# Kernel optimization log

Measured on AMD Instinct MI355X. Metric: run time of the kernel, lower is better.

Reference implementation:

```python
import jax, jax.numpy as jnp
import numpy as np

N_NODES = 100000


def _gcn_conv(x, W, b, src, dst, deg_inv_sqrt, n):
    # PyG GCNConv: h = x @ W; out[i] = sum_{(j->i)} norm_ji * h[j] + b
    h = x @ W                                   # [N, out_dim]
    norm = deg_inv_sqrt[src] * deg_inv_sqrt[dst]  # [E_total]
    msg = h[src] * norm[:, None]                # gather + scale
    out = jax.ops.segment_sum(msg, dst, num_segments=n)  # scatter-add
    return out + b


def setup_inputs() -> dict:
    key = jax.random.key(0)
    k1, k2, k3, k4, k5, k6 = jax.random.split(key, 6)
    num_features, hidden, embedding_size = 128, 32, 64
    n_edges = 3200000
    x = jax.random.normal(k1, (N_NODES, num_features), dtype=jnp.float32)
    edge_index = jax.random.randint(k2, (2, n_edges), 0, N_NODES, dtype=jnp.int64)
    # Glorot init like PyG GCNConv
    W1 = jax.random.normal(k3, (num_features, hidden), dtype=jnp.float32) * (1.0 / np.sqrt(num_features))
    b1 = jnp.zeros((hidden,), dtype=jnp.float32)
    W2 = jax.random.normal(k4, (hidden, embedding_size), dtype=jnp.float32) * (1.0 / np.sqrt(hidden))
    b2 = jnp.zeros((embedding_size,), dtype=jnp.float32)
    return {"x": x, "edge_index": edge_index, "W1": W1, "b1": b1, "W2": W2, "b2": b2}


def reference(x, edge_index, W1, b1, W2, b2):
    n = x.shape[0]
    # add self-loops (GCNConv default add_self_loops=True)
    loop = jnp.arange(n, dtype=edge_index.dtype)
    src = jnp.concatenate([edge_index[0], loop])
    dst = jnp.concatenate([edge_index[1], loop])
    # symmetric normalization: deg includes self-loops, edge_weight = 1
    deg = jax.ops.segment_sum(jnp.ones_like(dst, dtype=x.dtype), dst, num_segments=n)
    deg_inv_sqrt = jnp.where(deg > 0, jax.lax.rsqrt(deg), 0.0)

    h = _gcn_conv(x, W1, b1, src, dst, deg_inv_sqrt, n)
    h = jax.nn.relu(h)
    # F.dropout(p=0.2, training=False) -> identity in eval mode
    out = _gcn_conv(h, W2, b2, src, dst, deg_inv_sqrt, n)
    return out
```

## Files before the change

kernel.cpp:

```cpp
#include <hip/hip_runtime.h>
#include <hip/hip_bf16.h>


#define NF 128
#define HID 32
#define EMB 64

#define BSHIFT 10
#define BNODES 1024
#define CAPS 4608
#define CAP (8 * CAPS)
#define NBUKMAX 128
#define TILE 4096
#define EPT 16
#define CHUNKS 8

typedef float vf4 __attribute__((ext_vector_type(4)));
typedef unsigned vu4 __attribute__((ext_vector_type(4)));

static __device__ __forceinline__ unsigned bf16rne(float f) {
    unsigned u = __float_as_uint(f);
    return (u + 0x7fffu + ((u >> 16) & 1u)) >> 16;
}

static __device__ __host__ __forceinline__ int hslot(int b, int c) {
    return ((b >> 3) << 6) | (c << 3) | (b & 7);
}

#define ACC8(v) \
    a0 += __uint_as_float((v).x << 16); a1 += __uint_as_float((v).x & 0xffff0000u); \
    a2 += __uint_as_float((v).y << 16); a3 += __uint_as_float((v).y & 0xffff0000u); \
    a4 += __uint_as_float((v).z << 16); a5 += __uint_as_float((v).z & 0xffff0000u); \
    a6 += __uint_as_float((v).w << 16); a7 += __uint_as_float((v).w & 0xffff0000u);

__global__ __launch_bounds__(256) void k_part(const void* __restrict__ ei,
                                              unsigned* __restrict__ pairs,
                                              int* __restrict__ bcur8,
                                              int* __restrict__ cnt_ovf,
                                              unsigned long long* __restrict__ ovf,
                                              int* __restrict__ ovfcnt,
                                              int E, int nbuk) {
    __shared__ unsigned sEnt[TILE];
    __shared__ unsigned char sB[TILE];
    __shared__ int hcntw[4][NBUKMAX];
    __shared__ int lcurw[4][NBUKMAX];
    __shared__ int lstart[NBUKMAX], gbase[NBUKMAX];
    __shared__ int sNZ;
    const int tid = threadIdx.x;
    const int w = tid >> 6;
    const int grp = blockIdx.x & 7;
    const int tile0 = blockIdx.x * TILE;
    if (tile0 >= E) return;
    const int tcnt = min(TILE, E - tile0);

    if (tid == 0) sNZ = 0;
    for (int b = tid; b < 4 * NBUKMAX; b += 256) {
        ((int*)hcntw)[b] = 0;
        ((int*)lcurw)[b] = 0;
    }
    __syncthreads();
    {
        int i = tile0 + tid;
        if (i < E) {
            unsigned hw = ((const unsigned*)ei)[2 * (size_t)i + 1];
            if (hw) sNZ = 1;
        }
    }
    __syncthreads();
    const bool is64 = (sNZ == 0);

    int ms[EPT], md[EPT];
#pragma unroll
    for (int k = 0; k < EPT; ++k) {
        int i = tile0 + k * 256 + tid;
        ms[k] = -1;
        if (i < tile0 + tcnt) {
            int s, d;
            if (is64) {
                const long long* p = (const long long*)ei;
                s = (int)__builtin_nontemporal_load(&p[i]);
                d = (int)__builtin_nontemporal_load(&p[(size_t)E + i]);
            } else {
                const int* p = (const int*)ei;
                s = __builtin_nontemporal_load(&p[i]);
                d = __builtin_nontemporal_load(&p[E + i]);
            }
            ms[k] = s; md[k] = d;
            atomicAdd(&hcntw[w][d >> BSHIFT], 1);
        }
    }
    __syncthreads();

    if (tid < 64) {
        int i0 = tid * 2, i1 = tid * 2 + 1;
        int c0 = 0, c1 = 0;
        if (i0 < nbuk) { c0 = hcntw[0][i0] + hcntw[1][i0] + hcntw[2][i0] + hcntw[3][i0]; }
        if (i1 < nbuk) { c1 = hcntw[0][i1] + hcntw[1][i1] + hcntw[2][i1] + hcntw[3][i1]; }
        int run = c0 + c1, inc = run;
#pragma unroll
        for (int off = 1; off < 64; off <<= 1) {
            int t2 = __shfl_up(inc, off);
            if (tid >= off) inc += t2;
        }
        int excl = inc - run;
        if (i0 < nbuk) {
            lstart[i0] = excl;
            gbase[i0] = c0 ? atomicAdd(&bcur8[i0 * 8 + grp], c0) : 0;
            int off2 = excl;
#pragma unroll
            for (int ww = 0; ww < 4; ++ww) { int t3 = hcntw[ww][i0]; hcntw[ww][i0] = off2; off2 += t3; }
        }
        if (i1 < nbuk) {
            lstart[i1] = excl + c0;
            gbase[i1] = c1 ? atomicAdd(&bcur8[i1 * 8 + grp], c1) : 0;
            int off2 = excl + c0;
#pragma unroll
            for (int ww = 0; ww < 4; ++ww) { int t3 = hcntw[ww][i1]; hcntw[ww][i1] = off2; off2 += t3; }
        }
    }
    __syncthreads();

#pragma unroll
    for (int k = 0; k < EPT; ++k) {
        if (ms[k] >= 0) {
            int b = md[k] >> BSHIFT;
            int slot = hcntw[w][b] + atomicAdd(&lcurw[w][b], 1);
            sEnt[slot] = ((unsigned)(md[k] & (BNODES - 1)) << 17) | (unsigned)ms[k];
            sB[slot] = (unsigned char)b;
        }
    }
    __syncthreads();

    for (int j = tid; j < tcnt; j += 256) {
        unsigned ent = sEnt[j];
        int b = sB[j];
        int g = gbase[b] + (j - lstart[b]);
        if (g < CAPS) {
            pairs[(size_t)b * CAP + grp * CAPS + g] = ent;
        } else {
            int d = (b << BSHIFT) | (int)(ent >> 17);
            int s = (int)(ent & 0x1FFFFu);
            int o = atomicAdd(ovfcnt, 1);
            ovf[o] = ((unsigned long long)(unsigned)d << 32) | (unsigned)s;
            atomicAdd(&cnt_ovf[d], 1);
        }
    }
}

__global__ void k_bscan(const int* __restrict__ bcur8, int* __restrict__ bbase,
                        int* __restrict__ roff, int nbuk, int E, int N) {
    __shared__ int sh[128];
    int t = threadIdx.x;
    int v = 0;
    if (t < nbuk) {
#pragma unroll
        for (int k = 0; k < 8; ++k) v += bcur8[t * 8 + k];
    }
    sh[t] = v;
    __syncthreads();
    for (int off = 1; off < 128; off <<= 1) {
        int add = (t >= off) ? sh[t - off] : 0;
        __syncthreads();
        sh[t] += add;
        __syncthreads();
    }
    if (t < nbuk) bbase[t] = sh[t] - v;
    if (t == 0) roff[N] = E;
}

__global__ __launch_bounds__(256) void k_hist(const unsigned* __restrict__ pairs,
                                              const int* __restrict__ bcur8,
                                              int* __restrict__ histc, int nbuk) {
    __shared__ int hist[BNODES];
    const int idx = blockIdx.x;
    const int c = (idx >> 3) & 7;
    const int b = (idx & 7) | ((idx >> 6) << 3);
    if (b >= nbuk) return;
    const int tid = threadIdx.x;
    const int nbc = min(bcur8[b * 8 + c], CAPS);
    const int i0 = c * CAPS, i1 = i0 + nbc;
    const unsigned* pp = pairs + (size_t)b * CAP;
    for (int i = tid; i < BNODES; i += 256) hist[i] = 0;
    __syncthreads();
    for (int i = i0 + tid; i < i1; i += 256)
        atomicAdd(&hist[__builtin_nontemporal_load(&pp[i]) >> 17], 1);
    __syncthreads();
    int* outp = histc + ((size_t)idx << 10);
    for (int i = tid; i < BNODES; i += 256) outp[i] = hist[i];
}

__global__ __launch_bounds__(256) void k_nscan(int* __restrict__ histc,
                                               const int* __restrict__ bbase,
                                               const int* __restrict__ cnt_ovf,
                                               int* __restrict__ roff,
                                               int* __restrict__ cursor,
                                               float* __restrict__ dis, int N) {
    __shared__ int part[256];
    const int b = blockIdx.x, tid = threadIdx.x;
    const int base = bbase[b];
    int h[4][CHUNKS], stg[4], tv[4];
    int run = 0;
    const int l0 = tid * 4;
#pragma unroll
    for (int k = 0; k < 4; ++k) {
        int l = l0 + k;
        int node = (b << BSHIFT) + l;
        int st = 0;
#pragma unroll
        for (int c = 0; c < CHUNKS; ++c) {
            h[k][c] = histc[((size_t)hslot(b, c) << 10) + l];
            st += h[k][c];
        }
        stg[k] = st;
        int ov = (node < N) ? cnt_ovf[node] : 0;
        tv[k] = st + ov;
        run += tv[k];
    }
    part[tid] = run;
    __syncthreads();
    for (int off = 1; off < 256; off <<= 1) {
        int add = (tid >= off) ? part[tid - off] : 0;
        __syncthreads();
        part[tid] += add;
        __syncthreads();
    }
    int excl = part[tid] - run;
#pragma unroll
    for (int k = 0; k < 4; ++k) {
        int l = l0 + k;
        int node = (b << BSHIFT) + l;
        if (node < N) {
            roff[node] = base + excl;
            cursor[node] = base + excl + stg[k];
            dis[node] = rsqrtf((float)(tv[k] + 1));
        }
        int cb = base + excl;
#pragma unroll
        for (int c = 0; c < CHUNKS; ++c) {
            int hh = h[k][c];
            histc[((size_t)hslot(b, c) << 10) + l] = cb;
            cb += hh;
        }
        excl += tv[k];
    }
}

__global__ __launch_bounds__(256) void k_scat2(const unsigned* __restrict__ pairs,
                                               const int* __restrict__ bcur8,
                                               const int* __restrict__ histc,
                                               int* __restrict__ csr,
                                               const unsigned long long* __restrict__ ovf,
                                               const int* __restrict__ ovfcnt,
                                               int* __restrict__ cursor, int nbuk) {
    __shared__ int cbase[BNODES];
    __shared__ int lc[BNODES];
    const int idx = blockIdx.x;
    const int c = (idx >> 3) & 7;
    const int b = (idx & 7) | ((idx >> 6) << 3);
    const int tid = threadIdx.x;
    if (b < nbuk) {
        const int nbc = min(bcur8[b * 8 + c], CAPS);
        const int i0 = c * CAPS, i1 = i0 + nbc;
        const unsigned* pp = pairs + (size_t)b * CAP;
        const int* hc = histc + ((size_t)idx << 10);
        for (int i = tid; i < BNODES; i += 256) { cbase[i] = hc[i]; lc[i] = 0; }
        __syncthreads();
        int i = i0 + tid;
        for (; i + 768 < i1; i += 1024) {
            unsigned e0 = pp[i], e1 = pp[i + 256], e2 = pp[i + 512], e3 = pp[i + 768];
            int l0 = e0 >> 17, l1 = e1 >> 17, l2 = e2 >> 17, l3 = e3 >> 17;
            int p0 = cbase[l0] + atomicAdd(&lc[l0], 1);
            int p1 = cbase[l1] + atomicAdd(&lc[l1], 1);
            int p2 = cbase[l2] + atomicAdd(&lc[l2], 1);
            int p3 = cbase[l3] + atomicAdd(&lc[l3], 1);
            csr[p0] = (int)(e0 & 0x1FFFFu);
            csr[p1] = (int)(e1 & 0x1FFFFu);
            csr[p2] = (int)(e2 & 0x1FFFFu);
            csr[p3] = (int)(e3 & 0x1FFFFu);
        }
        for (; i < i1; i += 256) {
            unsigned ent = pp[i];
            int l = ent >> 17;
            int pos = cbase[l] + atomicAdd(&lc[l], 1);
            csr[pos] = (int)(ent & 0x1FFFFu);
        }
    }
    int n = *ovfcnt;
    for (int i = idx * 256 + tid; i < n; i += gridDim.x * 256) {
        unsigned long long pr = ovf[i];
        int pos = atomicAdd(&cursor[(int)(unsigned)(pr >> 32)], 1);
        csr[pos] = (int)(unsigned)pr;
    }
}

__global__ __launch_bounds__(256) void k_gemm1(const float* __restrict__ x,
                                               const float* __restrict__ W,
                                               const float* __restrict__ dis,
                                               unsigned* __restrict__ h1b, int N) {
    __shared__ float sW[NF * HID];
    __shared__ float sx[32][132];
    const int t = threadIdx.x;
    for (int i = t; i < NF * HID; i += 256) sW[i] = W[i];
    const int row0 = blockIdx.x * 32;
    {
        const float4* xv = (const float4*)(x + (size_t)row0 * NF);
        for (int i = t; i < 32 * 32; i += 256) {
            int r = i >> 5, c = i & 31;
            float4 v = make_float4(0.f, 0.f, 0.f, 0.f);
            if (row0 + r < N) v = xv[(size_t)r * 32 + c];
            *(float4*)&sx[r][c * 4] = v;
        }
    }
    __syncthreads();
    const int col4 = (t & 7) * 4;
    const int row = t >> 3;
    float a0 = 0.f, a1 = 0.f, a2 = 0.f, a3 = 0.f;
#pragma unroll 8
    for (int k = 0; k < NF; ++k) {
        float xs = sx[row][k];
        float4 w = *(const float4*)&sW[k * HID + col4];
        a0 += xs * w.x; a1 += xs * w.y; a2 += xs * w.z; a3 += xs * w.w;
    }
    int r = row0 + row;
    if (r < N) {
        float d = dis[r];
        unsigned u0 = bf16rne(a0 * d) | (bf16rne(a1 * d) << 16);
        unsigned u1 = bf16rne(a2 * d) | (bf16rne(a3 * d) << 16);
        *(uint2*)&h1b[(size_t)r * 16 + (t & 7) * 2] = make_uint2(u0, u1);
    }
}

__global__ __launch_bounds__(256) void k_agg1(const uint4* __restrict__ h1b,
                                              const int* __restrict__ roff,
                                              const int* __restrict__ csr,
                                              const float* __restrict__ dis,
                                              const float* __restrict__ b1,
                                              uint4* __restrict__ t_out, int N) {
    int tt = blockIdx.x * 256 + threadIdx.x;
    int node = tt >> 2;
    if (node >= N) return;
    int j = tt & 3;
    uint4 u = h1b[(size_t)node * 4 + j];
    float a0, a1, a2, a3, a4, a5, a6, a7;
    a0 = __uint_as_float(u.x << 16); a1 = __uint_as_float(u.x & 0xffff0000u);
    a2 = __uint_as_float(u.y << 16); a3 = __uint_as_float(u.y & 0xffff0000u);
    a4 = __uint_as_float(u.z << 16); a5 = __uint_as_float(u.z & 0xffff0000u);
    a6 = __uint_as_float(u.w << 16); a7 = __uint_as_float(u.w & 0xffff0000u);
    int e0 = roff[node], e1 = roff[node + 1];
    int e = e0;
    for (; e + 8 <= e1; e += 8) {
        int s0 = __builtin_nontemporal_load(&csr[e + 0]);
        int s1 = __builtin_nontemporal_load(&csr[e + 1]);
        int s2 = __builtin_nontemporal_load(&csr[e + 2]);
        int s3 = __builtin_nontemporal_load(&csr[e + 3]);
        int s4 = __builtin_nontemporal_load(&csr[e + 4]);
        int s5 = __builtin_nontemporal_load(&csr[e + 5]);
        int s6 = __builtin_nontemporal_load(&csr[e + 6]);
        int s7 = __builtin_nontemporal_load(&csr[e + 7]);
        uint4 v0 = h1b[(size_t)s0 * 4 + j];
        uint4 v1 = h1b[(size_t)s1 * 4 + j];
        uint4 v2 = h1b[(size_t)s2 * 4 + j];
        uint4 v3 = h1b[(size_t)s3 * 4 + j];
        uint4 v4 = h1b[(size_t)s4 * 4 + j];
        uint4 v5 = h1b[(size_t)s5 * 4 + j];
        uint4 v6 = h1b[(size_t)s6 * 4 + j];
        uint4 v7 = h1b[(size_t)s7 * 4 + j];
        ACC8(v0) ACC8(v1) ACC8(v2) ACC8(v3) ACC8(v4) ACC8(v5) ACC8(v6) ACC8(v7)
    }
    for (; e + 4 <= e1; e += 4) {
        int s0 = __builtin_nontemporal_load(&csr[e + 0]);
        int s1 = __builtin_nontemporal_load(&csr[e + 1]);
        int s2 = __builtin_nontemporal_load(&csr[e + 2]);
        int s3 = __builtin_nontemporal_load(&csr[e + 3]);
        uint4 v0 = h1b[(size_t)s0 * 4 + j];
        uint4 v1 = h1b[(size_t)s1 * 4 + j];
        uint4 v2 = h1b[(size_t)s2 * 4 + j];
        uint4 v3 = h1b[(size_t)s3 * 4 + j];
        ACC8(v0) ACC8(v1) ACC8(v2) ACC8(v3)
    }
    for (; e < e1; ++e) {
        int s = __builtin_nontemporal_load(&csr[e]);
        uint4 v = h1b[(size_t)s * 4 + j];
        ACC8(v)
    }
    float d = dis[node];
    float4 bb0 = *(const float4*)&b1[j * 8];
    float4 bb1 = *(const float4*)&b1[j * 8 + 4];
    float r0 = fmaxf(a0 * d + bb0.x, 0.f) * d, r1 = fmaxf(a1 * d + bb0.y, 0.f) * d;
    float r2 = fmaxf(a2 * d + bb0.z, 0.f) * d, r3 = fmaxf(a3 * d + bb0.w, 0.f) * d;
    float r4 = fmaxf(a4 * d + bb1.x, 0.f) * d, r5 = fmaxf(a5 * d + bb1.y, 0.f) * d;
    float r6 = fmaxf(a6 * d + bb1.z, 0.f) * d, r7 = fmaxf(a7 * d + bb1.w, 0.f) * d;
    uint4 o;
    o.x = bf16rne(r0) | (bf16rne(r1) << 16);
    o.y = bf16rne(r2) | (bf16rne(r3) << 16);
    o.z = bf16rne(r4) | (bf16rne(r5) << 16);
    o.w = bf16rne(r6) | (bf16rne(r7) << 16);
    t_out[(size_t)node * 4 + j] = o;
}

__global__ __launch_bounds__(256) void k_agg2(const uint4* __restrict__ tb,
                                              const int* __restrict__ roff,
                                              const int* __restrict__ csr,
                                              const float* __restrict__ dis,
                                              float* __restrict__ s2, int N) {
    int tt = blockIdx.x * 256 + threadIdx.x;
    int node = tt >> 2;
    if (node >= N) return;
    int j = tt & 3;
    uint4 u = tb[(size_t)node * 4 + j];
    float a0, a1, a2, a3, a4, a5, a6, a7;
    a0 = __uint_as_float(u.x << 16); a1 = __uint_as_float(u.x & 0xffff0000u);
    a2 = __uint_as_float(u.y << 16); a3 = __uint_as_float(u.y & 0xffff0000u);
    a4 = __uint_as_float(u.z << 16); a5 = __uint_as_float(u.z & 0xffff0000u);
    a6 = __uint_as_float(u.w << 16); a7 = __uint_as_float(u.w & 0xffff0000u);
    int e0 = roff[node], e1 = roff[node + 1];
    int e = e0;
    for (; e + 8 <= e1; e += 8) {
        int s0 = __builtin_nontemporal_load(&csr[e + 0]);
        int s1 = __builtin_nontemporal_load(&csr[e + 1]);
        int s2i = __builtin_nontemporal_load(&csr[e + 2]);
        int s3 = __builtin_nontemporal_load(&csr[e + 3]);
        int s4 = __builtin_nontemporal_load(&csr[e + 4]);
        int s5 = __builtin_nontemporal_load(&csr[e + 5]);
        int s6 = __builtin_nontemporal_load(&csr[e + 6]);
        int s7 = __builtin_nontemporal_load(&csr[e + 7]);
        uint4 v0 = tb[(size_t)s0 * 4 + j];
        uint4 v1 = tb[(size_t)s1 * 4 + j];
        uint4 v2 = tb[(size_t)s2i * 4 + j];
        uint4 v3 = tb[(size_t)s3 * 4 + j];
        uint4 v4 = tb[(size_t)s4 * 4 + j];
        uint4 v5 = tb[(size_t)s5 * 4 + j];
        uint4 v6 = tb[(size_t)s6 * 4 + j];
        uint4 v7 = tb[(size_t)s7 * 4 + j];
        ACC8(v0) ACC8(v1) ACC8(v2) ACC8(v3) ACC8(v4) ACC8(v5) ACC8(v6) ACC8(v7)
    }
    for (; e + 4 <= e1; e += 4) {
        int s0 = __builtin_nontemporal_load(&csr[e + 0]);
        int s1 = __builtin_nontemporal_load(&csr[e + 1]);
        int s2i = __builtin_nontemporal_load(&csr[e + 2]);
        int s3 = __builtin_nontemporal_load(&csr[e + 3]);
        uint4 v0 = tb[(size_t)s0 * 4 + j];
        uint4 v1 = tb[(size_t)s1 * 4 + j];
        uint4 v2 = tb[(size_t)s2i * 4 + j];
        uint4 v3 = tb[(size_t)s3 * 4 + j];
        ACC8(v0) ACC8(v1) ACC8(v2) ACC8(v3)
    }
    for (; e < e1; ++e) {
        int s = __builtin_nontemporal_load(&csr[e]);
        uint4 v = tb[(size_t)s * 4 + j];
        ACC8(v)
    }
    float d = dis[node];
    vf4 o0, o1;
    o0.x = a0 * d; o0.y = a1 * d; o0.z = a2 * d; o0.w = a3 * d;
    o1.x = a4 * d; o1.y = a5 * d; o1.z = a6 * d; o1.w = a7 * d;
    vf4* op = (vf4*)&s2[(size_t)node * HID + j * 8];
    __builtin_nontemporal_store(o0, op);
    __builtin_nontemporal_store(o1, op + 1);
}

__global__ __launch_bounds__(256) void k_gemm2(const float* __restrict__ a,
                                               const float* __restrict__ W,
                                               const float* __restrict__ b2,
                                               float* __restrict__ out, int N) {
    __shared__ float sW[HID * EMB];
    __shared__ float sx[32][36];
    const int t = threadIdx.x;
    for (int i = t; i < HID * EMB; i += 256) sW[i] = W[i];
    const int row0 = blockIdx.x * 32;
    {
        const float4* av = (const float4*)(a + (size_t)row0 * HID);
        int r = t >> 3, c = t & 7;
        float4 v = make_float4(0.f, 0.f, 0.f, 0.f);
        if (row0 + r < N) v = av[(size_t)r * 8 + c];
        *(float4*)&sx[r][c * 4] = v;
    }
    __syncthreads();
    const int col4 = (t & 15) * 4;
    const int r0 = t >> 4;
    float a00 = 0.f, a01 = 0.f, a02 = 0.f, a03 = 0.f;
    float a10 = 0.f, a11 = 0.f, a12 = 0.f, a13 = 0.f;
#pragma unroll
    for (int k = 0; k < HID; ++k) {
        float4 w = *(const float4*)&sW[k * EMB + col4];
        float xa = sx[r0][k];
        float xb = sx[r0 + 16][k];
        a00 += xa * w.x; a01 += xa * w.y; a02 += xa * w.z; a03 += xa * w.w;
        a10 += xb * w.x; a11 += xb * w.y; a12 += xb * w.z; a13 += xb * w.w;
    }
    float4 bb = *(const float4*)&b2[col4];
    int ra = row0 + r0, rb = row0 + r0 + 16;
    if (ra < N) {
        vf4 o; o.x = a00 + bb.x; o.y = a01 + bb.y; o.z = a02 + bb.z; o.w = a03 + bb.w;
        __builtin_nontemporal_store(o, (vf4*)&out[(size_t)ra * EMB + col4]);
    }
    if (rb < N) {
        vf4 o; o.x = a10 + bb.x; o.y = a11 + bb.y; o.z = a12 + bb.z; o.w = a13 + bb.w;
        __builtin_nontemporal_store(o, (vf4*)&out[(size_t)rb * EMB + col4]);
    }
}

extern "C" void kernel_launch(void* const* d_in, const int* in_sizes, int n_in,
                              void* d_out, int out_size, void* d_ws, size_t ws_size,
                              hipStream_t stream) {
    const float* x  = (const float*)d_in[0];
    const void*  ei = d_in[1];
    const float* W1 = (const float*)d_in[2];
    const float* b1 = (const float*)d_in[3];
    const float* W2 = (const float*)d_in[4];
    const float* b2 = (const float*)d_in[5];
    float* out = (float*)d_out;

    const int N = in_sizes[0] / NF;
    const int E = in_sizes[1] / 2;
    const int nbuk = (N + BNODES - 1) >> BSHIFT;

    char* ws = (char*)d_ws;
    size_t off = 0;
    auto take = [&](size_t bytes) -> void* {
        void* p = ws + off;
        off += (bytes + 255) & ~(size_t)255;
        return p;
    };
    int* cnt_ovf = (int*)take((size_t)N * 4);
    int* bcur8   = (int*)take((size_t)NBUKMAX * 8 * 4);
    int* ovfcnt  = (int*)take(4);
    size_t zbytes = off;
    int*                bbase  = (int*)take((size_t)NBUKMAX * 4);
    int*                roff   = (int*)take((size_t)(N + 1) * 4);
    int*                cursor = (int*)take((size_t)N * 4);
    float*              dis    = (float*)take((size_t)N * 4);
    int*                histc  = (int*)take((size_t)NBUKMAX * CHUNKS * BNODES * 4);
    unsigned*           pairs  = (unsigned*)take((size_t)nbuk * CAP * 4);
    unsigned long long* ovf    = (unsigned long long*)take((size_t)E * 8);
    int*                csr    = (int*)take((size_t)E * 4);
    unsigned*           h1b    = (unsigned*)take((size_t)N * HID * 2);
    unsigned*           tb     = (unsigned*)take((size_t)N * HID * 2);
    float*              s2     = (float*)take((size_t)N * HID * 4);

    (void)hipMemsetAsync(cnt_ovf, 0, zbytes, stream);

    const int gridBC = ((nbuk + 7) / 8) * 64;
    const int gridAgg = (int)(((size_t)N * 4 + 255) / 256);

    k_part<<<(E + TILE - 1) / TILE, 256, 0, stream>>>(ei, pairs, bcur8, cnt_ovf,
                                                      ovf, ovfcnt, E, nbuk);
    k_bscan<<<1, 128, 0, stream>>>(bcur8, bbase, roff, nbuk, E, N);
    k_hist<<<gridBC, 256, 0, stream>>>(pairs, bcur8, histc, nbuk);
    k_nscan<<<nbuk, 256, 0, stream>>>(histc, bbase, cnt_ovf, roff, cursor, dis, N);
    k_scat2<<<gridBC, 256, 0, stream>>>(pairs, bcur8, histc, csr, ovf, ovfcnt,
                                        cursor, nbuk);

    k_gemm1<<<(N + 31) / 32, 256, 0, stream>>>(x, W1, dis, h1b, N);
    k_agg1<<<gridAgg, 256, 0, stream>>>((const uint4*)h1b, roff, csr, dis, b1,
                                        (uint4*)tb, N);
    k_agg2<<<gridAgg, 256, 0, stream>>>((const uint4*)tb, roff, csr, dis, s2, N);
    k_gemm2<<<(N + 31) / 32, 256, 0, stream>>>(s2, W2, b2, out, N);
}
```

Baseline: 231.6 us.

## Fuse second aggregation with output GEMM and simplify partition slot atomics

Merges the layer-2 aggregation kernel and the 32x64 output GEMM into one kernel. Aggregated rows are staged in shared memory and multiplied by W2 in the same block, which removes the s2 intermediate write and read and one launch. It also drops the separate lcurw counter array in the partition kernel by doing atomicAdd directly on the prefix-offset array. The fused kernel now loads W2 into shared memory in every aggregation block and adds a block barrier after the irregular gather loop.

```diff
diff --git a/kernel.cpp b/kernel.cpp
--- a/kernel.cpp
+++ b/kernel.cpp
@@ -43,7 +43,6 @@
     __shared__ unsigned sEnt[TILE];
     __shared__ unsigned char sB[TILE];
     __shared__ int hcntw[4][NBUKMAX];
-    __shared__ int lcurw[4][NBUKMAX];
     __shared__ int lstart[NBUKMAX], gbase[NBUKMAX];
     __shared__ int sNZ;
     const int tid = threadIdx.x;
@@ -54,10 +53,7 @@
     const int tcnt = min(TILE, E - tile0);
 
     if (tid == 0) sNZ = 0;
-    for (int b = tid; b < 4 * NBUKMAX; b += 256) {
-        ((int*)hcntw)[b] = 0;
-        ((int*)lcurw)[b] = 0;
-    }
+    for (int b = tid; b < 4 * NBUKMAX; b += 256) ((int*)hcntw)[b] = 0;
     __syncthreads();
     {
         int i = tile0 + tid;
@@ -124,7 +120,7 @@
     for (int k = 0; k < EPT; ++k) {
         if (ms[k] >= 0) {
             int b = md[k] >> BSHIFT;
-            int slot = hcntw[w][b] + atomicAdd(&lcurw[w][b], 1);
+            int slot = atomicAdd(&hcntw[w][b], 1);
             sEnt[slot] = ((unsigned)(md[k] & (BNODES - 1)) << 17) | (unsigned)ms[k];
             sB[slot] = (unsigned char)b;
         }
@@ -398,105 +394,98 @@
     t_out[(size_t)node * 4 + j] = o;
 }
 
-__global__ __launch_bounds__(256) void k_agg2(const uint4* __restrict__ tb,
-                                              const int* __restrict__ roff,
-                                              const int* __restrict__ csr,
-                                              const float* __restrict__ dis,
-                                              float* __restrict__ s2, int N) {
-    int tt = blockIdx.x * 256 + threadIdx.x;
-    int node = tt >> 2;
-    if (node >= N) return;
-    int j = tt & 3;
-    uint4 u = tb[(size_t)node * 4 + j];
-    float a0, a1, a2, a3, a4, a5, a6, a7;
-    a0 = __uint_as_float(u.x << 16); a1 = __uint_as_float(u.x & 0xffff0000u);
-    a2 = __uint_as_float(u.y << 16); a3 = __uint_as_float(u.y & 0xffff0000u);
-    a4 = __uint_as_float(u.z << 16); a5 = __uint_as_float(u.z & 0xffff0000u);
-    a6 = __uint_as_float(u.w << 16); a7 = __uint_as_float(u.w & 0xffff0000u);
-    int e0 = roff[node], e1 = roff[node + 1];
-    int e = e0;
-    for (; e + 8 <= e1; e += 8) {
-        int s0 = __builtin_nontemporal_load(&csr[e + 0]);
-        int s1 = __builtin_nontemporal_load(&csr[e + 1]);
-        int s2i = __builtin_nontemporal_load(&csr[e + 2]);
-        int s3 = __builtin_nontemporal_load(&csr[e + 3]);
-        int s4 = __builtin_nontemporal_load(&csr[e + 4]);
-        int s5 = __builtin_nontemporal_load(&csr[e + 5]);
-        int s6 = __builtin_nontemporal_load(&csr[e + 6]);
-        int s7 = __builtin_nontemporal_load(&csr[e + 7]);
-        uint4 v0 = tb[(size_t)s0 * 4 + j];
-        uint4 v1 = tb[(size_t)s1 * 4 + j];
-        uint4 v2 = tb[(size_t)s2i * 4 + j];
-        uint4 v3 = tb[(size_t)s3 * 4 + j];
-        uint4 v4 = tb[(size_t)s4 * 4 + j];
-        uint4 v5 = tb[(size_t)s5 * 4 + j];
-        uint4 v6 = tb[(size_t)s6 * 4 + j];
-        uint4 v7 = tb[(size_t)s7 * 4 + j];
-        ACC8(v0) ACC8(v1) ACC8(v2) ACC8(v3) ACC8(v4) ACC8(v5) ACC8(v6) ACC8(v7)
-    }
-    for (; e + 4 <= e1; e += 4) {
-        int s0 = __builtin_nontemporal_load(&csr[e + 0]);
-        int s1 = __builtin_nontemporal_load(&csr[e + 1]);
-        int s2i = __builtin_nontemporal_load(&csr[e + 2]);
-        int s3 = __builtin_nontemporal_load(&csr[e + 3]);
-        uint4 v0 = tb[(size_t)s0 * 4 + j];
-        uint4 v1 = tb[(size_t)s1 * 4 + j];
-        uint4 v2 = tb[(size_t)s2i * 4 + j];
-        uint4 v3 = tb[(size_t)s3 * 4 + j];
-        ACC8(v0) ACC8(v1) ACC8(v2) ACC8(v3)
-    }
-    for (; e < e1; ++e) {
-        int s = __builtin_nontemporal_load(&csr[e]);
-        uint4 v = tb[(size_t)s * 4 + j];
-        ACC8(v)
-    }
-    float d = dis[node];
-    vf4 o0, o1;
-    o0.x = a0 * d; o0.y = a1 * d; o0.z = a2 * d; o0.w = a3 * d;
-    o1.x = a4 * d; o1.y = a5 * d; o1.z = a6 * d; o1.w = a7 * d;
-    vf4* op = (vf4*)&s2[(size_t)node * HID + j * 8];
-    __builtin_nontemporal_store(o0, op);
-    __builtin_nontemporal_store(o1, op + 1);
-}
-
-__global__ __launch_bounds__(256) void k_gemm2(const float* __restrict__ a,
-                                               const float* __restrict__ W,
+__global__ __launch_bounds__(256) void k_agg2f(const uint4* __restrict__ tb,
+                                               const int* __restrict__ roff,
+                                               const int* __restrict__ csr,
+                                               const float* __restrict__ dis,
+                                               const float* __restrict__ W2,
                                                const float* __restrict__ b2,
                                                float* __restrict__ out, int N) {
     __shared__ float sW[HID * EMB];
-    __shared__ float sx[32][36];
-    const int t = threadIdx.x;
-    for (int i = t; i < HID * EMB; i += 256) sW[i] = W[i];
-    const int row0 = blockIdx.x * 32;
-    {
-        const float4* av = (const float4*)(a + (size_t)row0 * HID);
-        int r = t >> 3, c = t & 7;
-        float4 v = make_float4(0.f, 0.f, 0.f, 0.f);
-        if (row0 + r < N) v = av[(size_t)r * 8 + c];
-        *(float4*)&sx[r][c * 4] = v;
-    }
-    __syncthreads();
-    const int col4 = (t & 15) * 4;
-    const int r0 = t >> 4;
-    float a00 = 0.f, a01 = 0.f, a02 = 0.f, a03 = 0.f;
-    float a10 = 0.f, a11 = 0.f, a12 = 0.f, a13 = 0.f;
-#pragma unroll
-    for (int k = 0; k < HID; ++k) {
-        float4 w = *(const float4*)&sW[k * EMB + col4];
-        float xa = sx[r0][k];
-        float xb = sx[r0 + 16][k];
-        a00 += xa * w.x; a01 += xa * w.y; a02 += xa * w.z; a03 += xa * w.w;
-        a10 += xb * w.x; a11 += xb * w.y; a12 += xb * w.z; a13 += xb * w.w;
-    }
-    float4 bb = *(const float4*)&b2[col4];
-    int ra = row0 + r0, rb = row0 + r0 + 16;
-    if (ra < N) {
-        vf4 o; o.x = a00 + bb.x; o.y = a01 + bb.y; o.z = a02 + bb.z; o.w = a03 + bb.w;
-        __builtin_nontemporal_store(o, (vf4*)&out[(size_t)ra * EMB + col4]);
-    }
-    if (rb < N) {
-        vf4 o; o.x = a10 + bb.x; o.y = a11 + bb.y; o.z = a12 + bb.z; o.w = a13 + bb.w;
-        __builtin_nontemporal_store(o, (vf4*)&out[(size_t)rb * EMB + col4]);
+    __shared__ float sS[64][33];
+    const int tid = threadIdx.x;
+    for (int i = tid; i < HID * EMB; i += 256) sW[i] = W2[i];
+    int tt = blockIdx.x * 256 + tid;
+    int node = tt >> 2;
+    int j = tt & 3;
+    int nl = tid >> 2;
+    bool valid = (node < N);
+    if (valid) {
+        uint4 u = tb[(size_t)node * 4 + j];
+        float a0, a1, a2, a3, a4, a5, a6, a7;
+        a0 = __uint_as_float(u.x << 16); a1 = __uint_as_float(u.x & 0xffff0000u);
+        a2 = __uint_as_float(u.y << 16); a3 = __uint_as_float(u.y & 0xffff0000u);
+        a4 = __uint_as_float(u.z << 16); a5 = __uint_as_float(u.z & 0xffff0000u);
+        a6 = __uint_as_float(u.w << 16); a7 = __uint_as_float(u.w & 0xffff0000u);
+        int e0 = roff[node], e1 = roff[node + 1];
+        int e = e0;
+        for (; e + 8 <= e1; e += 8) {
+            int s0 = __builtin_nontemporal_load(&csr[e + 0]);
+            int s1 = __builtin_nontemporal_load(&csr[e + 1]);
+            int s2i = __builtin_nontemporal_load(&csr[e + 2]);
+            int s3 = __builtin_nontemporal_load(&csr[e + 3]);
+            int s4 = __builtin_nontemporal_load(&csr[e + 4]);
+            int s5 = __builtin_nontemporal_load(&csr[e + 5]);
+            int s6 = __builtin_nontemporal_load(&csr[e + 6]);
+            int s7 = __builtin_nontemporal_load(&csr[e + 7]);
+            uint4 v0 = tb[(size_t)s0 * 4 + j];
+            uint4 v1 = tb[(size_t)s1 * 4 + j];
+            uint4 v2 = tb[(size_t)s2i * 4 + j];
+            uint4 v3 = tb[(size_t)s3 * 4 + j];
+            uint4 v4 = tb[(size_t)s4 * 4 + j];
+            uint4 v5 = tb[(size_t)s5 * 4 + j];
+            uint4 v6 = tb[(size_t)s6 * 4 + j];
+            uint4 v7 = tb[(size_t)s7 * 4 + j];
+            ACC8(v0) ACC8(v1) ACC8(v2) ACC8(v3) ACC8(v4) ACC8(v5) ACC8(v6) ACC8(v7)
+        }
+        for (; e + 4 <= e1; e += 4) {
+            int s0 = __builtin_nontemporal_load(&csr[e + 0]);
+            int s1 = __builtin_nontemporal_load(&csr[e + 1]);
+            int s2i = __builtin_nontemporal_load(&csr[e + 2]);
+            int s3 = __builtin_nontemporal_load(&csr[e + 3]);
+            uint4 v0 = tb[(size_t)s0 * 4 + j];
+            uint4 v1 = tb[(size_t)s1 * 4 + j];
+            uint4 v2 = tb[(size_t)s2i * 4 + j];
+            uint4 v3 = tb[(size_t)s3 * 4 + j];
+            ACC8(v0) ACC8(v1) ACC8(v2) ACC8(v3)
+        }
+        for (; e < e1; ++e) {
+            int s = __builtin_nontemporal_load(&csr[e]);
+            uint4 v = tb[(size_t)s * 4 + j];
+            ACC8(v)
+        }
+        float d = dis[node];
+        float* sp = &sS[nl][j * 8];
+        sp[0] = a0 * d; sp[1] = a1 * d; sp[2] = a2 * d; sp[3] = a3 * d;
+        sp[4] = a4 * d; sp[5] = a5 * d; sp[6] = a6 * d; sp[7] = a7 * d;
+    }
+    __syncthreads();
+    if (valid) {
+        const int cb = j * 16;
+        float4 c0 = *(const float4*)&b2[cb];
+        float4 c1 = *(const float4*)&b2[cb + 4];
+        float4 c2 = *(const float4*)&b2[cb + 8];
+        float4 c3 = *(const float4*)&b2[cb + 12];
+#pragma unroll 8
+        for (int k = 0; k < HID; ++k) {
+            float s = sS[nl][k];
+            const float4* w = (const float4*)&sW[k * EMB + cb];
+            float4 w0 = w[0], w1 = w[1], w2 = w[2], w3 = w[3];
+            c0.x += s * w0.x; c0.y += s * w0.y; c0.z += s * w0.z; c0.w += s * w0.w;
+            c1.x += s * w1.x; c1.y += s * w1.y; c1.z += s * w1.z; c1.w += s * w1.w;
+            c2.x += s * w2.x; c2.y += s * w2.y; c2.z += s * w2.z; c2.w += s * w2.w;
+            c3.x += s * w3.x; c3.y += s * w3.y; c3.z += s * w3.z; c3.w += s * w3.w;
+        }
+        float* op = &out[(size_t)node * EMB + cb];
+        vf4 o0, o1, o2, o3;
+        o0.x = c0.x; o0.y = c0.y; o0.z = c0.z; o0.w = c0.w;
+        o1.x = c1.x; o1.y = c1.y; o1.z = c1.z; o1.w = c1.w;
+        o2.x = c2.x; o2.y = c2.y; o2.z = c2.z; o2.w = c2.w;
+        o3.x = c3.x; o3.y = c3.y; o3.z = c3.z; o3.w = c3.w;
+        __builtin_nontemporal_store(o0, (vf4*)op);
+        __builtin_nontemporal_store(o1, (vf4*)(op + 4));
+        __builtin_nontemporal_store(o2, (vf4*)(op + 8));
+        __builtin_nontemporal_store(o3, (vf4*)(op + 12));
     }
 }
 
@@ -536,7 +525,6 @@
     int*                csr    = (int*)take((size_t)E * 4);
     unsigned*           h1b    = (unsigned*)take((size_t)N * HID * 2);
     unsigned*           tb     = (unsigned*)take((size_t)N * HID * 2);
-    float*              s2     = (float*)take((size_t)N * HID * 4);
 
     (void)hipMemsetAsync(cnt_ovf, 0, zbytes, stream);
 
@@ -554,6 +542,6 @@
     k_gemm1<<<(N + 31) / 32, 256, 0, stream>>>(x, W1, dis, h1b, N);
     k_agg1<<<gridAgg, 256, 0, stream>>>((const uint4*)h1b, roff, csr, dis, b1,
                                         (uint4*)tb, N);
-    k_agg2<<<gridAgg, 256, 0, stream>>>((const uint4*)tb, roff, csr, dis, s2, N);
-    k_gemm2<<<(N + 31) / 32, 256, 0, stream>>>(s2, W2, b2, out, N);
-}
+    k_agg2f<<<gridAgg, 256, 0, stream>>>((const uint4*)tb, roff, csr, dis,
+                                         W2, b2, out, N);
+}
```

Result: faster. 221.6 us (-4.3%).
